# Optimization experiments

Measured on AMD Instinct MI355X. Metric: run time of the kernel, lower is better.

The kernel has to match this reference:

```python
import jax, jax.numpy as jnp
import numpy as np

GOP = 4

def _resize_bilinear(x, Ho, Wo):
    # x: (M, C, Hs, Ws); matches F.interpolate(mode='bilinear', align_corners=False)
    M, C, Hs, Ws = x.shape
    ys = jnp.clip((jnp.arange(Ho, dtype=jnp.float32) + 0.5) * (Hs / Ho) - 0.5, 0.0, Hs - 1.0)
    xs = jnp.clip((jnp.arange(Wo, dtype=jnp.float32) + 0.5) * (Ws / Wo) - 0.5, 0.0, Ws - 1.0)
    y0 = jnp.floor(ys).astype(jnp.int32); y1 = jnp.minimum(y0 + 1, Hs - 1)
    x0 = jnp.floor(xs).astype(jnp.int32); x1 = jnp.minimum(x0 + 1, Ws - 1)
    wy = (ys - y0)[None, None, :, None]
    wx = (xs - x0)[None, None, None, :]
    r0 = x[:, :, y0, :]; r1 = x[:, :, y1, :]
    top = r0[:, :, :, x0] * (1 - wx) + r0[:, :, :, x1] * wx
    bot = r1[:, :, :, x0] * (1 - wx) + r1[:, :, :, x1] * wx
    return top * (1 - wy) + bot * wy

def _deform_sample(feat, flow):
    # feat: (M,C,H,W); flow: (M,2,H,W), ch0=dy, ch1=dx (torchvision deform_conv order).
    # Bilinear sample at (y+dy, x+dx) with zero padding outside (kernel_size=1 deform conv).
    M, C, H, W = feat.shape
    gy = jnp.arange(H, dtype=flow.dtype)[:, None]
    gx = jnp.arange(W, dtype=flow.dtype)[None, :]
    y = gy + flow[:, 0]; x = gx + flow[:, 1]          # (M,H,W)
    y0f = jnp.floor(y); x0f = jnp.floor(x)
    wy = (y - y0f)[:, None]; wx = (x - x0f)[:, None]  # (M,1,H,W)
    y0 = y0f.astype(jnp.int32); x0 = x0f.astype(jnp.int32)
    feat_flat = feat.reshape(M, C, H * W)
    def gather(yi, xi):
        valid = ((yi >= 0) & (yi < H) & (xi >= 0) & (xi < W)).astype(feat.dtype)
        idx = (jnp.clip(yi, 0, H - 1) * W + jnp.clip(xi, 0, W - 1)).reshape(M, H * W)
        v = jnp.take_along_axis(feat_flat, jnp.broadcast_to(idx[:, None, :], (M, C, H * W)), axis=2)
        return v.reshape(M, C, H, W) * valid[:, None]
    v00 = gather(y0, x0);     v01 = gather(y0, x0 + 1)
    v10 = gather(y0 + 1, x0); v11 = gather(y0 + 1, x0 + 1)
    return v00 * (1 - wy) * (1 - wx) + v01 * (1 - wy) * wx + v10 * wy * (1 - wx) + v11 * wy * wx

def setup_inputs():
    key = jax.random.key(0)
    k = jax.random.split(key, 7)
    B, T, Himg, Wimg = 4, 16, 256, 256
    num_gop = T // GOP      # 4
    t = GOP - 1             # 3 P-frames per GOP
    C_in, D, h, w = 256, 256, 64, 64
    imgs = jnp.zeros((B, T, 3, Himg, Wimg), jnp.float32)
    i_features = jax.random.normal(k[0], (B * num_gop, C_in, h, w), jnp.float32)
    # flows of a few pixels at image scale (scaled by 0.25 inside forward)
    p_motions = jax.random.normal(k[1], (B, num_gop * t, 2, Himg, Wimg), jnp.float32) * 8.0
    W_emb = jax.random.normal(k[2], (D, C_in), jnp.float32) * 0.02
    b_emb = jax.random.normal(k[3], (D,), jnp.float32) * 0.02
    W_dc = jax.random.normal(k[4], (D, D), jnp.float32) * 0.02
    b_dc = jax.random.normal(k[5], (D,), jnp.float32) * 0.02
    return {"imgs": imgs, "i_features": i_features, "p_motions": p_motions,
            "W_emb": W_emb, "b_emb": b_emb, "W_dc": W_dc, "b_dc": b_dc}

def reference(imgs, i_features, p_motions, W_emb, b_emb, W_dc, b_dc):
    B = imgs.shape[0]
    num_gop = imgs.shape[1] // GOP
    # 1x1 embedding conv
    feat = jnp.einsum('mchw,oc->mohw', i_features, W_emb) + b_emb[None, :, None, None]
    M0, D, h, w = feat.shape
    scale = w / imgs.shape[-1]
    Tp = p_motions.shape[1]
    flow = _resize_bilinear(p_motions.reshape(B * Tp, 2, p_motions.shape[-2], p_motions.shape[-1]), h, w) * scale
    t = Tp // num_gop
    # repeat each GOP's I-frame features for its t P-frame flows
    feat = jnp.broadcast_to(feat.reshape(B, num_gop, 1, D, h, w), (B, num_gop, t, D, h, w)).reshape(-1, D, h, w)
    flow = flow.reshape(-1, 2, h, w)
    # flow-guided deformable conv with 1x1 kernel: bilinear gather + 1x1 projection
    samp = _deform_sample(feat, flow)
    out = jnp.einsum('mchw,oc->mohw', samp, W_dc) + b_dc[None, :, None, None]
    # adaptive_avg_pool2d(.,1).flatten(3)
    return out.mean(axis=(-2, -1)).reshape(B, num_gop, t, D)
```

## Files before the change

kernel.cpp:

```cpp
#include <hip/hip_runtime.h>
#include <math.h>

#define HW 4096
#define CIN 256
#define DD 256
#define M_TOTAL 48
#define NSP 4
#define SPPX (HW / NSP)

__global__ __launch_bounds__(256) void k_pre(
    const float* __restrict__ p_motions,
    const float* __restrict__ W_emb,
    const float* __restrict__ b_emb,
    const float* __restrict__ W_dc,
    float* __restrict__ Ag4,
    float* __restrict__ Sg4,
    float* __restrict__ WT,
    float* __restrict__ bfold,
    float* __restrict__ out)
{
    const int tid = threadIdx.x;
    const int bid = blockIdx.x;

    if (bid < M_TOTAL * NSP) {
        __shared__ float Al[HW];
        __shared__ float red[4];
        const int m = bid >> 2;
        const int sp = bid & 3;
        const float4* p0 = (const float4*)(p_motions + (size_t)m * 2 * 65536);
        const float4* p1 = p0 + 65536 / 4;

        for (int i = tid; i < HW; i += 256) Al[i] = 0.f;
        __syncthreads();

        #pragma unroll
        for (int ii = 0; ii < SPPX / 256; ++ii) {
            const int i = ii * 256 + tid;
            const int y = sp * 16 + (i >> 6);
            const int x = i & 63;
            const int r1 = 4 * y + 1, r2 = 4 * y + 2;
            const float4 v10 = p0[r1 * 64 + x];
            const float4 v20 = p0[r2 * 64 + x];
            const float4 v11 = p1[r1 * 64 + x];
            const float4 v21 = p1[r2 * 64 + x];
            const float fy = (v10.y + v10.z + v20.y + v20.z) * 0.0625f;
            const float fx = (v11.y + v11.z + v21.y + v21.z) * 0.0625f;

            const float yy = (float)y + fy;
            const float xx = (float)x + fx;
            const float y0f = floorf(yy), x0f = floorf(xx);
            const float wy = yy - y0f, wx = xx - x0f;
            const int iy0 = (int)y0f, ix0 = (int)x0f;
            const int iy1 = iy0 + 1, ix1 = ix0 + 1;
            const float w00 = (1.f - wy) * (1.f - wx);
            const float w01 = (1.f - wy) * wx;
            const float w10 = wy * (1.f - wx);
            const float w11 = wy * wx;
            const bool y0ok = (iy0 >= 0) & (iy0 < 64);
            const bool y1ok = (iy1 >= 0) & (iy1 < 64);
            const bool x0ok = (ix0 >= 0) & (ix0 < 64);
            const bool x1ok = (ix1 >= 0) & (ix1 < 64);
            if (y0ok & x0ok) atomicAdd(&Al[iy0 * 64 + ix0], w00);
            if (y0ok & x1ok) atomicAdd(&Al[iy0 * 64 + ix1], w01);
            if (y1ok & x0ok) atomicAdd(&Al[iy1 * 64 + ix0], w10);
            if (y1ok & x1ok) atomicAdd(&Al[iy1 * 64 + ix1], w11);
        }
        __syncthreads();

        const float4* Al4 = (const float4*)Al;
        float4* dst = (float4*)(Ag4 + (size_t)(m * NSP + sp) * HW);
        float part = 0.f;
        #pragma unroll
        for (int i = tid; i < HW / 4; i += 256) {
            const float4 v = Al4[i];
            dst[i] = v;
            part += v.x + v.y + v.z + v.w;
        }
        for (int off = 32; off > 0; off >>= 1) part += __shfl_down(part, off, 64);
        if ((tid & 63) == 0) red[tid >> 6] = part;
        __syncthreads();
        if (tid == 0) Sg4[m * NSP + sp] = red[0] + red[1] + red[2] + red[3];
    } else {
        __shared__ float wdc[256];
        __shared__ float red2[4];
        const int o = bid - M_TOTAL * NSP;
        wdc[tid] = W_dc[(size_t)o * 256 + tid];
        if (tid < 48) out[(size_t)o * 48 + tid] = 0.f;
        __syncthreads();
        float acc = 0.f;
        #pragma unroll 8
        for (int k = 0; k < 256; ++k)
            acc += wdc[k] * W_emb[(size_t)k * 256 + tid];
        WT[(size_t)tid * 256 + o] = acc;

        float pb = wdc[tid] * b_emb[tid];
        for (int off = 32; off > 0; off >>= 1) pb += __shfl_down(pb, off, 64);
        if ((tid & 63) == 0) red2[tid >> 6] = pb;
        __syncthreads();
        if (tid == 0) bfold[o] = red2[0] + red2[1] + red2[2] + red2[3];
    }
}

__global__ __launch_bounds__(256, 4) void k_gather_out(
    const float* __restrict__ i_features,
    const float* __restrict__ Ag4,
    const float* __restrict__ Sg4,
    const float* __restrict__ WT,
    const float* __restrict__ bfold,
    const float* __restrict__ b_dc,
    float* __restrict__ out)
{
    __shared__ float gl[3][16];
    const int fm = blockIdx.x;
    const int chunk = blockIdx.y;
    const int sp = blockIdx.z;
    const int tid = threadIdx.x;
    const int wave = tid >> 6, lane = tid & 63;
    const int m0 = fm * 3;

    float4 a[3][4];
    #pragma unroll
    for (int j = 0; j < 3; ++j) {
        const float4* P0 = (const float4*)(Ag4 + ((size_t)((m0 + j) * NSP + 0)) * HW + sp * SPPX);
        const float4* P1 = (const float4*)(Ag4 + ((size_t)((m0 + j) * NSP + 1)) * HW + sp * SPPX);
        const float4* P2 = (const float4*)(Ag4 + ((size_t)((m0 + j) * NSP + 2)) * HW + sp * SPPX);
        const float4* P3 = (const float4*)(Ag4 + ((size_t)((m0 + j) * NSP + 3)) * HW + sp * SPPX);
        #pragma unroll
        for (int k = 0; k < 4; ++k) {
            const float4 t0 = P0[lane + 64 * k];
            const float4 t1 = P1[lane + 64 * k];
            const float4 t2 = P2[lane + 64 * k];
            const float4 t3 = P3[lane + 64 * k];
            a[j][k].x = t0.x + t1.x + t2.x + t3.x;
            a[j][k].y = t0.y + t1.y + t2.y + t3.y;
            a[j][k].z = t0.z + t1.z + t2.z + t3.z;
            a[j][k].w = t0.w + t1.w + t2.w + t3.w;
        }
    }

    #pragma unroll
    for (int c = 0; c < 4; ++c) {
        const int ci = chunk * 16 + wave * 4 + c;
        const float4* f4 = (const float4*)(i_features + ((size_t)fm * CIN + ci) * HW + sp * SPPX);
        float s0 = 0.f, s1 = 0.f, s2 = 0.f;
        #pragma unroll
        for (int k = 0; k < 4; ++k) {
            const float4 v = f4[lane + 64 * k];
            s0 += v.x * a[0][k].x + v.y * a[0][k].y + v.z * a[0][k].z + v.w * a[0][k].w;
            s1 += v.x * a[1][k].x + v.y * a[1][k].y + v.z * a[1][k].z + v.w * a[1][k].w;
            s2 += v.x * a[2][k].x + v.y * a[2][k].y + v.z * a[2][k].z + v.w * a[2][k].w;
        }
        #pragma unroll
        for (int off = 32; off > 0; off >>= 1) {
            s0 += __shfl_down(s0, off, 64);
            s1 += __shfl_down(s1, off, 64);
            s2 += __shfl_down(s2, off, 64);
        }
        if (lane == 0) {
            gl[0][wave * 4 + c] = s0;
            gl[1][wave * 4 + c] = s1;
            gl[2][wave * 4 + c] = s2;
        }
    }
    __syncthreads();

    const int o = tid;
    float acc0 = 0.f, acc1 = 0.f, acc2 = 0.f;
    #pragma unroll
    for (int q = 0; q < 16; ++q) {
        const float wv = WT[(size_t)(chunk * 16 + q) * DD + o];
        acc0 += gl[0][q] * wv;
        acc1 += gl[1][q] * wv;
        acc2 += gl[2][q] * wv;
    }
    const float inv = 1.f / 4096.f;
    atomicAdd(&out[(size_t)(m0 + 0) * DD + o], acc0 * inv);
    atomicAdd(&out[(size_t)(m0 + 1) * DD + o], acc1 * inv);
    atomicAdd(&out[(size_t)(m0 + 2) * DD + o], acc2 * inv);

    if (chunk == 0 && sp == 0) {
        #pragma unroll
        for (int j = 0; j < 3; ++j) {
            const int m = m0 + j;
            const float Sm = (Sg4[m * NSP + 0] + Sg4[m * NSP + 1] +
                              Sg4[m * NSP + 2] + Sg4[m * NSP + 3]) * inv;
            atomicAdd(&out[(size_t)m * DD + tid], bfold[tid] * Sm + b_dc[tid]);
        }
    }
}

extern "C" void kernel_launch(void* const* d_in, const int* in_sizes, int n_in,
                              void* d_out, int out_size, void* d_ws, size_t ws_size,
                              hipStream_t stream) {
    const float* i_features = (const float*)d_in[1];
    const float* p_motions  = (const float*)d_in[2];
    const float* W_emb      = (const float*)d_in[3];
    const float* b_emb      = (const float*)d_in[4];
    const float* W_dc       = (const float*)d_in[5];
    const float* b_dc       = (const float*)d_in[6];
    float* out = (float*)d_out;

    float* ws = (float*)d_ws;
    float* Ag4   = ws;
    float* Sg4   = Ag4 + (size_t)M_TOTAL * NSP * HW;
    float* WT    = Sg4 + 256;
    float* bfold = WT + 65536;

    k_pre<<<M_TOTAL * NSP + DD, 256, 0, stream>>>(p_motions, W_emb, b_emb, W_dc,
                                                  Ag4, Sg4, WT, bfold, out);
    dim3 g2(16, 16, NSP);
    k_gather_out<<<g2, 256, 0, stream>>>(i_features, Ag4, Sg4, WT, bfold, b_dc, out);
}
```

Measured before the change: 162.4 us.

## Halve spatial split in gather kernel and stage summed weights through shared memory

The gather kernel now splits each frame's pixels into two parts instead of four, so each block covers twice as many pixels. The four partial weight maps are summed cooperatively by all 256 threads into shared memory rather than redundantly by each wave. Each wave then loads its 24 float4 weights from shared memory. The aim is to cut duplicated global reads of Ag4 and halve the per-output atomics, at the cost of higher register pressure (launch bounds lowered to 2 blocks per CU), fewer blocks in flight, and an extra barrier.

```diff
diff --git a/kernel.cpp b/kernel.cpp
--- a/kernel.cpp
+++ b/kernel.cpp
@@ -6,7 +6,8 @@
 #define DD 256
 #define M_TOTAL 48
 #define NSP 4
-#define SPPX (HW / NSP)
+#define KSP 2
+#define KPX (HW / KSP)
 
 __global__ __launch_bounds__(256) void k_pre(
     const float* __restrict__ p_motions,
@@ -34,7 +35,7 @@
         __syncthreads();
 
         #pragma unroll
-        for (int ii = 0; ii < SPPX / 256; ++ii) {
+        for (int ii = 0; ii < (HW / NSP) / 256; ++ii) {
             const int i = ii * 256 + tid;
             const int y = sp * 16 + (i >> 6);
             const int x = i & 63;
@@ -101,7 +102,7 @@
     }
 }
 
-__global__ __launch_bounds__(256, 4) void k_gather_out(
+__global__ __launch_bounds__(256, 2) void k_gather_out(
     const float* __restrict__ i_features,
     const float* __restrict__ Ag4,
     const float* __restrict__ Sg4,
@@ -110,6 +111,7 @@
     const float* __restrict__ b_dc,
     float* __restrict__ out)
 {
+    __shared__ float As[3 * KPX];
     __shared__ float gl[3][16];
     const int fm = blockIdx.x;
     const int chunk = blockIdx.y;
@@ -118,33 +120,40 @@
     const int wave = tid >> 6, lane = tid & 63;
     const int m0 = fm * 3;
 
-    float4 a[3][4];
+    float4* As4 = (float4*)As;
     #pragma unroll
     for (int j = 0; j < 3; ++j) {
-        const float4* P0 = (const float4*)(Ag4 + ((size_t)((m0 + j) * NSP + 0)) * HW + sp * SPPX);
-        const float4* P1 = (const float4*)(Ag4 + ((size_t)((m0 + j) * NSP + 1)) * HW + sp * SPPX);
-        const float4* P2 = (const float4*)(Ag4 + ((size_t)((m0 + j) * NSP + 2)) * HW + sp * SPPX);
-        const float4* P3 = (const float4*)(Ag4 + ((size_t)((m0 + j) * NSP + 3)) * HW + sp * SPPX);
-        #pragma unroll
-        for (int k = 0; k < 4; ++k) {
-            const float4 t0 = P0[lane + 64 * k];
-            const float4 t1 = P1[lane + 64 * k];
-            const float4 t2 = P2[lane + 64 * k];
-            const float4 t3 = P3[lane + 64 * k];
-            a[j][k].x = t0.x + t1.x + t2.x + t3.x;
-            a[j][k].y = t0.y + t1.y + t2.y + t3.y;
-            a[j][k].z = t0.z + t1.z + t2.z + t3.z;
-            a[j][k].w = t0.w + t1.w + t2.w + t3.w;
-        }
-    }
-
+        const float4* P = (const float4*)(Ag4 + ((size_t)((m0 + j) * NSP)) * HW + sp * KPX);
+        #pragma unroll
+        for (int t = 0; t < KPX / 4; t += 256) {
+            const float4 t0 = P[t + tid];
+            const float4 t1 = P[t + tid + 1 * (HW / 4)];
+            const float4 t2 = P[t + tid + 2 * (HW / 4)];
+            const float4 t3 = P[t + tid + 3 * (HW / 4)];
+            float4 s;
+            s.x = t0.x + t1.x + t2.x + t3.x;
+            s.y = t0.y + t1.y + t2.y + t3.y;
+            s.z = t0.z + t1.z + t2.z + t3.z;
+            s.w = t0.w + t1.w + t2.w + t3.w;
+            As4[j * (KPX / 4) + t + tid] = s;
+        }
+    }
+    __syncthreads();
+
+    float4 a[3][8];
     #pragma unroll
+    for (int j = 0; j < 3; ++j)
+        #pragma unroll
+        for (int k = 0; k < 8; ++k)
+            a[j][k] = As4[j * (KPX / 4) + lane + 64 * k];
+
+    #pragma unroll 2
     for (int c = 0; c < 4; ++c) {
         const int ci = chunk * 16 + wave * 4 + c;
-        const float4* f4 = (const float4*)(i_features + ((size_t)fm * CIN + ci) * HW + sp * SPPX);
+        const float4* f4 = (const float4*)(i_features + ((size_t)fm * CIN + ci) * HW + sp * KPX);
         float s0 = 0.f, s1 = 0.f, s2 = 0.f;
         #pragma unroll
-        for (int k = 0; k < 4; ++k) {
+        for (int k = 0; k < 8; ++k) {
             const float4 v = f4[lane + 64 * k];
             s0 += v.x * a[0][k].x + v.y * a[0][k].y + v.z * a[0][k].z + v.w * a[0][k].w;
             s1 += v.x * a[1][k].x + v.y * a[1][k].y + v.z * a[1][k].z + v.w * a[1][k].w;
@@ -208,6 +217,6 @@
 
     k_pre<<<M_TOTAL * NSP + DD, 256, 0, stream>>>(p_motions, W_emb, b_emb, W_dc,
                                                   Ag4, Sg4, WT, bfold, out);
-    dim3 g2(16, 16, NSP);
+    dim3 g2(16, 16, KSP);
     k_gather_out<<<g2, 256, 0, stream>>>(i_features, Ag4, Sg4, WT, bfold, b_dc, out);
 }
```

Result: slower. 170.7 us (+5.1%).
